# Kernel tuning notes

Measured on AMD Instinct MI355X. Metric: run time of the kernel, lower is better.

## Reference

```python
import jax, jax.numpy as jnp
import numpy as np

DIM = 192; HEADS = 6; WS = 8; SHIFT = 4; HID = int(DIM * 4.0)
CAB_SCALE = 0.01; COMPRESS = 3; SQUEEZE = 30
B = 8; H0 = 128; W0 = 128


def window_partition(x, ws):
    Bn, H, W, C = x.shape
    x = x.reshape(Bn, H // ws, ws, W // ws, ws, C).transpose(0, 1, 3, 2, 4, 5)
    return x.reshape(-1, ws, ws, C)


def window_reverse(w, ws, H, W):
    Bn = w.shape[0] // ((H // ws) * (W // ws))
    x = w.reshape(Bn, H // ws, W // ws, ws, ws, -1).transpose(0, 1, 3, 2, 4, 5)
    return x.reshape(Bn, H, W, -1)


def layernorm(x, w, b):
    mu = jnp.mean(x, -1, keepdims=True)
    var = jnp.var(x, -1, keepdims=True)
    return (x - mu) * jax.lax.rsqrt(var + 1e-5) * w + b


def conv3x3(x, w, b):
    y = jax.lax.conv_general_dilated(x, w, (1, 1), [(1, 1), (1, 1)],
                                     dimension_numbers=('NCHW', 'OIHW', 'NCHW'))
    return y + b[None, :, None, None]


def _coords_table(ws):
    # continuous relative coords table, log-spaced as in SwinV2
    r = np.arange(-(ws - 1), ws, dtype=np.float32)
    t = np.stack(np.meshgrid(r, r, indexing='ij'), -1) / (ws - 1) * 8.0
    t = np.sign(t) * np.log2(np.abs(t) + 1.0) / np.log2(8.0)
    return jnp.asarray(t.reshape(-1, 2))  # ((2ws-1)^2, 2)


def _rel_index(ws):
    c = np.stack(np.meshgrid(np.arange(ws), np.arange(ws), indexing='ij')).reshape(2, -1)
    r = (c[:, :, None] - c[:, None, :]).transpose(1, 2, 0)
    r[..., 0] += ws - 1; r[..., 1] += ws - 1; r[..., 0] *= 2 * ws - 1
    return jnp.asarray(r.sum(-1))  # (N, N) int


def _attn_mask(H, W, ws, shift):
    img = np.zeros((1, H, W, 1), np.float32); cnt = 0
    for hs in (slice(0, -ws), slice(-ws, -shift), slice(-shift, None)):
        for wsl in (slice(0, -ws), slice(-ws, -shift), slice(-shift, None)):
            img[:, hs, wsl, :] = cnt; cnt += 1
    win = img.reshape(1, H // ws, ws, W // ws, ws, 1).transpose(0, 1, 3, 2, 4, 5).reshape(-1, ws * ws)
    m = win[:, None, :] - win[:, :, None]
    return jnp.asarray(np.where(m != 0, -100.0, 0.0).astype(np.float32))  # (nW, N, N)


def _forward(x, norm1_w, norm1_b, qkv_w, q_bias, v_bias, logit_scale,
             cpb_w1, cpb_b1, cpb_w2, proj_w, proj_b,
             cab1_w, cab1_b, cab2_w, cab2_b, ca1_w, ca1_b, ca2_w, ca2_b,
             norm2_w, norm2_b, fc1_w, fc1_b, fc2_w, fc2_b, H, W):
    Bn, L, C = x.shape
    nh = HEADS; hd = C // nh; N = WS * WS
    shortcut = x
    xn = layernorm(x, norm1_w, norm1_b)
    xi = xn.reshape(Bn, H, W, C)

    # ---- CAB branch (Conv-GELU-Conv + channel attention) ----
    xc = xi.transpose(0, 3, 1, 2)                      # NCHW
    c = conv3x3(xc, cab1_w, cab1_b)
    c = jax.nn.gelu(c, approximate=False)
    c = conv3x3(c, cab2_w, cab2_b)
    s = c.mean((2, 3))                                 # (B, C) squeeze
    s = jax.nn.relu(s @ ca1_w.T + ca1_b)
    s = jax.nn.sigmoid(s @ ca2_w.T + ca2_b)
    conv_x = (c * s[:, :, None, None]).transpose(0, 2, 3, 1).reshape(Bn, L, C)

    # ---- shifted-window cosine attention ----
    xs = jnp.roll(xi, (-SHIFT, -SHIFT), axis=(1, 2)) if SHIFT > 0 else xi
    xw = window_partition(xs, WS).reshape(-1, N, C)    # (B*nW, N, C)
    qkv_bias = jnp.concatenate([q_bias, jnp.zeros_like(v_bias), v_bias])
    qkv = (xw @ qkv_w.T + qkv_bias).reshape(-1, N, 3, nh, hd).transpose(2, 0, 3, 1, 4)
    q, k, v = qkv[0], qkv[1], qkv[2]                   # (B_, nh, N, hd)
    qn = q / jnp.maximum(jnp.linalg.norm(q, axis=-1, keepdims=True), 1e-12)
    kn = k / jnp.maximum(jnp.linalg.norm(k, axis=-1, keepdims=True), 1e-12)
    attn = jnp.einsum('bhnd,bhmd->bhnm', qn, kn)
    scale = jnp.exp(jnp.minimum(logit_scale, jnp.log(100.0)))  # (nh,1,1)
    attn = attn * scale
    # CPB MLP relative position bias
    hbias = jax.nn.relu(_coords_table(WS) @ cpb_w1.T + cpb_b1) @ cpb_w2.T  # (T, nh)
    rpb = hbias[_rel_index(WS).reshape(-1)].reshape(N, N, nh).transpose(2, 0, 1)
    attn = attn + 16.0 * jax.nn.sigmoid(rpb)[None]
    if SHIFT > 0:
        mask = _attn_mask(H, W, WS, SHIFT)             # (nW, N, N)
        nW = mask.shape[0]
        attn = (attn.reshape(-1, nW, nh, N, N) + mask[None, :, None]).reshape(-1, nh, N, N)
    attn = jax.nn.softmax(attn, axis=-1)
    out = jnp.einsum('bhnm,bhmd->bhnd', attn, v).transpose(0, 2, 1, 3).reshape(-1, N, C)
    out = out @ proj_w.T + proj_b
    out = window_reverse(out.reshape(-1, WS, WS, C), WS, H, W)
    if SHIFT > 0:
        out = jnp.roll(out, (SHIFT, SHIFT), axis=(1, 2))
    attn_x = out.reshape(Bn, L, C)

    x = shortcut + attn_x + CAB_SCALE * conv_x
    h = layernorm(x, norm2_w, norm2_b)
    h = jax.nn.gelu(h @ fc1_w.T + fc1_b, approximate=False) @ fc2_w.T + fc2_b
    return x + h


def setup_inputs() -> dict:
    key = jax.random.key(0)
    ks = jax.random.split(key, 24)
    r = lambda k, shp, s=0.02: (jax.random.normal(k, shp, jnp.float32) * s)
    C = DIM; Cc = DIM // COMPRESS; Cs = DIM // SQUEEZE
    return {
        'x': jax.random.normal(ks[0], (B, H0 * W0, C), jnp.float32),
        'H': H0, 'W': W0,
        'norm1_w': jnp.ones((C,), jnp.float32), 'norm1_b': jnp.zeros((C,), jnp.float32),
        'qkv_w': r(ks[1], (3 * C, C)),
        'q_bias': jnp.zeros((C,), jnp.float32), 'v_bias': jnp.zeros((C,), jnp.float32),
        'logit_scale': jnp.full((HEADS, 1, 1), np.log(10.0), jnp.float32),
        'cpb_w1': r(ks[2], (512, 2), 0.1), 'cpb_b1': jnp.zeros((512,), jnp.float32),
        'cpb_w2': r(ks[3], (HEADS, 512), 0.1),
        'proj_w': r(ks[4], (C, C)), 'proj_b': jnp.zeros((C,), jnp.float32),
        'cab1_w': r(ks[5], (Cc, C, 3, 3)), 'cab1_b': jnp.zeros((Cc,), jnp.float32),
        'cab2_w': r(ks[6], (C, Cc, 3, 3)), 'cab2_b': jnp.zeros((C,), jnp.float32),
        'ca1_w': r(ks[7], (Cs, C)), 'ca1_b': jnp.zeros((Cs,), jnp.float32),
        'ca2_w': r(ks[8], (C, Cs)), 'ca2_b': jnp.zeros((C,), jnp.float32),
        'norm2_w': jnp.ones((C,), jnp.float32), 'norm2_b': jnp.zeros((C,), jnp.float32),
        'fc1_w': r(ks[9], (HID, C)), 'fc1_b': jnp.zeros((HID,), jnp.float32),
        'fc2_w': r(ks[10], (C, HID)), 'fc2_b': jnp.zeros((C,), jnp.float32),
    }


def reference(x, H, W, norm1_w, norm1_b, qkv_w, q_bias, v_bias, logit_scale,
              cpb_w1, cpb_b1, cpb_w2, proj_w, proj_b,
              cab1_w, cab1_b, cab2_w, cab2_b, ca1_w, ca1_b, ca2_w, ca2_b,
              norm2_w, norm2_b, fc1_w, fc1_b, fc2_w, fc2_b):
    return _forward(x, norm1_w, norm1_b, qkv_w, q_bias, v_bias, logit_scale,
                    cpb_w1, cpb_b1, cpb_w2, proj_w, proj_b,
                    cab1_w, cab1_b, cab2_w, cab2_b, ca1_w, ca1_b, ca2_w, ca2_b,
                    norm2_w, norm2_b, fc1_w, fc1_b, fc2_w, fc2_b, int(H), int(W))
```

## Files before the change

kernel.cpp:

```cpp
#include <hip/hip_runtime.h>
#include <math.h>


typedef unsigned short u16;
typedef __attribute__((ext_vector_type(8))) short short8;
typedef __attribute__((ext_vector_type(4))) float f32x4;

#define DI static __device__ __forceinline__

DI float b2f(u16 u){ union{unsigned u; float f;} v; v.u = ((unsigned)u)<<16; return v.f; }
DI u16 f2b(float f){ union{float f; unsigned u;} v; v.f = f; unsigned r = v.u + 0x7fffu + ((v.u>>16)&1u); return (u16)(r>>16); }
DI float gelu_f(float x){
  const float u = x*(0.7978845608f + 0.0356774081f*x*x);
  const float r = __builtin_amdgcn_rcpf(1.0f + __expf(2.0f*u));
  return x - x*r;
}

#define C2PLANE (12582912L)

__global__ __launch_bounds__(256) void ln_k(const float* __restrict__ in,
    const float* __restrict__ w, const float* __restrict__ b, u16* __restrict__ out)
{
  const int row  = blockIdx.x*4 + (threadIdx.x>>6);
  const int lane = threadIdx.x & 63;
  const float* r = in + (long)row*192;
  float v0 = r[lane], v1 = r[lane+64], v2 = r[lane+128];
  float s = v0+v1+v2;
  #pragma unroll
  for (int m=1;m<64;m<<=1) s += __shfl_xor(s, m);
  float mu = s*(1.0f/192.0f);
  float d0=v0-mu, d1=v1-mu, d2=v2-mu;
  float q = d0*d0+d1*d1+d2*d2;
  #pragma unroll
  for (int m=1;m<64;m<<=1) q += __shfl_xor(q, m);
  float rstd = rsqrtf(q*(1.0f/192.0f)+1e-5f);
  u16* o = out + (long)row*192;
  o[lane]     = f2b(d0*rstd*w[lane]    +b[lane]);
  o[lane+64]  = f2b(d1*rstd*w[lane+64] +b[lane+64]);
  o[lane+128] = f2b(d2*rstd*w[lane+128]+b[lane+128]);
}

__global__ __launch_bounds__(256) void prep_k(
    const float* __restrict__ qkv_w, const float* __restrict__ q_bias,
    const float* __restrict__ v_bias, const float* __restrict__ proj_w,
    const float* __restrict__ fc1_w, const float* __restrict__ fc2_w,
    const float* __restrict__ cab1_w, const float* __restrict__ cab2_w,
    const float* __restrict__ lgs,
    float* __restrict__ qkvbias, u16* __restrict__ wqkv, u16* __restrict__ wproj,
    u16* __restrict__ wfc1, u16* __restrict__ wfc2, u16* __restrict__ wt1,
    u16* __restrict__ wt2, float* __restrict__ scale6)
{
  int o = blockIdx.x*256 + threadIdx.x;
  if (o < 576){ qkvbias[o] = (o<192)? q_bias[o] : ((o<384)? 0.f : v_bias[o-384]); return; }
  o -= 576;
  if (o < 110592){ wqkv[o] = f2b(qkv_w[o]); return; } o -= 110592;
  if (o < 36864){
    const int e = o&7, lane = (o>>3)&63, ks = (o>>9)%6, nr = o/3072;
    const int row = nr*16 + (lane&15), col = ks*32 + (lane>>4)*8 + e;
    wproj[o] = f2b(proj_w[row*192 + col]); return; } o -= 36864;
  if (o < 147456){
    const int e = o&7, lane = (o>>3)&63, ks = (o>>9)%6, rest = o/3072;
    const int nr = rest&3, p = rest>>2;
    const int row = p*64 + nr*16 + (lane&15), col = ks*32 + (lane>>4)*8 + e;
    wfc1[o] = f2b(fc1_w[row*192 + col]); return; } o -= 147456;
  if (o < 147456){
    const int e = o&7, lane = (o>>3)&63, ks2 = (o>>9)&1, rest = o>>10;
    const int nr2 = rest%12, p = rest/12;
    const int row = nr2*16 + (lane&15);
    const int col = p*64 + ks2*32 + (lane>>4)*8 + e;
    wfc2[o] = f2b(fc2_w[row*768 + col]); return; } o -= 147456;
  if (o < 110592){
    int s = o/12288, r = o%12288, oc = r/192, ic = r%192, kh = s/3, kw = s%3;
    wt1[o] = f2b(cab1_w[((oc*192+ic)*3+kh)*3+kw]); return; } o -= 110592;
  if (o < 110592){
    int s = o/12288, r = o%12288, oc = r/64, ic = r%64, kh = s/3, kw = s%3;
    wt2[o] = f2b(cab2_w[((oc*64+ic)*3+kh)*3+kw]); return; } o -= 110592;
  if (o < 6){ scale6[o] = expf(fminf(lgs[o], logf(100.f))); }
}

__global__ __launch_bounds__(256) void rpb_k(const float* __restrict__ w1,
    const float* __restrict__ b1, const float* __restrict__ w2, float* __restrict__ rpbL)
{
  __shared__ float hb[225*6];
  const int tid = threadIdx.x;
  if (tid < 225){
    int di = tid/15, dj = tid%15;
    float vi = (di-7)*(8.0f/7.0f), vj = (dj-7)*(8.0f/7.0f);
    float t0 = (vi==0.f)?0.f:copysignf(log2f(fabsf(vi)+1.f)*(1.f/3.f), vi);
    float t1 = (vj==0.f)?0.f:copysignf(log2f(fabsf(vj)+1.f)*(1.f/3.f), vj);
    float acc[6] = {0,0,0,0,0,0};
    for (int hd=0; hd<512; ++hd){
      float a = fmaxf(t0*w1[hd*2] + t1*w1[hd*2+1] + b1[hd], 0.f);
      #pragma unroll
      for (int h=0;h<6;++h) acc[h] += a*w2[h*512+hd];
    }
    #pragma unroll
    for (int h=0;h<6;++h) hb[tid*6+h] = acc[h];
  }
  __syncthreads();
  for (int o = tid; o < 24576; o += 256){
    int i = o&3, lane = (o>>2)&63, mK = (o>>8)&3, nQ = (o>>10)&3, h = o>>12;
    int q = nQ*16 + (lane&15), k = mK*16 + (lane>>4)*4 + i;
    int idx = ((q>>3)-(k>>3)+7)*15 + ((q&7)-(k&7)+7);
    rpbL[o] = 16.0f/(1.0f+expf(-hb[idx*6+h]));
  }
}

template<int EPI, int KK, int NN>
__global__ __launch_bounds__(256) void gemm4_k(
    const u16* __restrict__ A, const u16* __restrict__ W,
    const float* __restrict__ bias, u16* __restrict__ outb)
{
  constexpr int NP = NN/64;
  __shared__ __align__(16) u16 As[128*200];
  __shared__ __align__(16) u16 Bs[64*200];
  const int tid = threadIdx.x, w = tid>>6, lane = tid&63;
  const int fr = lane&15, g = lane>>4;
  const int m0 = blockIdx.x*128;
  u16* obuf = Bs;

  #pragma unroll
  for (int i=0;i<12;++i){ const int id=tid+i*256, row=id/24, cc=id%24;
    *(short8*)&As[row*200+cc*8] =
      *(const short8*)(A + (long)(m0+row)*KK + cc*8); }

  short8 breg[6];
  #define LOADB(p) { \
    _Pragma("unroll") \
    for (int i=0;i<6;++i){ const int id=tid+i*256, br=id/24, cc=id%24; \
      breg[i] = *(const short8*)(W + (long)((p)*64+br)*KK + cc*8); } }
  #define STOREB() { \
    _Pragma("unroll") \
    for (int i=0;i<6;++i){ const int id=tid+i*256, br=id/24, cc=id%24; \
      *(short8*)&Bs[br*200+cc*8] = breg[i]; } }

  LOADB(0);
  for (int p=0; p<NP; ++p){
    __syncthreads();
    STOREB();
    __syncthreads();
    if (p+1 < NP) LOADB(p+1);
    f32x4 acc[2][4];
    #pragma unroll
    for (int a=0;a<2;++a)
      #pragma unroll
      for (int b=0;b<4;++b) acc[a][b] = (f32x4){0.f,0.f,0.f,0.f};
    #pragma unroll
    for (int ks=0; ks<6; ++ks){
      short8 af0 = *(const short8*)&As[(w*32+   fr)*200 + ks*32 + g*8];
      short8 af1 = *(const short8*)&As[(w*32+16+fr)*200 + ks*32 + g*8];
      #pragma unroll
      for (int nr=0;nr<4;++nr){
        short8 bf = *(const short8*)&Bs[(nr*16+fr)*200 + ks*32 + g*8];
        acc[0][nr] = __builtin_amdgcn_mfma_f32_16x16x32_bf16(af0, bf, acc[0][nr], 0,0,0);
        acc[1][nr] = __builtin_amdgcn_mfma_f32_16x16x32_bf16(af1, bf, acc[1][nr], 0,0,0);
      } }
    __syncthreads();
    #pragma unroll
    for (int mr=0;mr<2;++mr)
      #pragma unroll
      for (int nr=0;nr<4;++nr){
        const float bc = bias[p*64+nr*16+fr];
        #pragma unroll
        for (int i=0;i<4;++i){
          const int tok = w*32+mr*16+g*4+i;
          obuf[tok*72 + nr*16+fr] = f2b(acc[mr][nr][i] + bc); } }
    __syncthreads();
    #pragma unroll
    for (int j=0;j<4;++j){
      const int idx = tid + j*256, tok = idx>>3, cc = idx&7;
      *(short8*)(outb + (long)(m0+tok)*NN + p*64 + cc*8) =
          *(const short8*)&obuf[tok*72 + cc*8]; }
  }
  #undef LOADB
  #undef STOREB
}

__global__ __launch_bounds__(256) void proj_k(
    const u16* __restrict__ A, const u16* __restrict__ W,
    const float* __restrict__ bias, const float* __restrict__ resx,
    const u16* __restrict__ c2in, const float* __restrict__ sgate,
    float* __restrict__ outf)
{
  __shared__ __align__(16) u16 As[64*200];
  const int tid = threadIdx.x, w = tid>>6, lane = tid&63;
  const int fr = lane&15, g = lane>>4;
  const int m0 = blockIdx.x*64;

  #pragma unroll
  for (int i=0;i<6;++i){ const int id=tid+i*256, r=id/24, cc=id%24;
    *(short8*)&As[r*200+cc*8] = *(const short8*)(A + (long)(m0+r)*192 + cc*8); }
  __syncthreads();

  f32x4 acc[12];
  #pragma unroll
  for (int n=0;n<12;++n) acc[n] = (f32x4){0.f,0.f,0.f,0.f};
  #pragma unroll
  for (int ks=0;ks<6;++ks){
    const short8 af = *(const short8*)&As[(w*16+fr)*200 + ks*32 + g*8];
    #pragma unroll
    for (int nr=0;nr<12;++nr){
      const short8 bf = *(const short8*)(W + ((nr*6+ks)*64 + lane)*8);
      acc[nr] = __builtin_amdgcn_mfma_f32_16x16x32_bf16(af, bf, acc[nr], 0,0,0);
    }
  }

  float* fbuf = (float*)As;
  #pragma unroll
  for (int ch=0;ch<2;++ch){
    __syncthreads();
    #pragma unroll
    for (int nr=0;nr<6;++nr){
      const float bc = bias[ch*96 + nr*16 + fr];
      #pragma unroll
      for (int i=0;i<4;++i)
        fbuf[(w*16+g*4+i)*100 + nr*16+fr] = acc[ch*6+nr][i] + bc;
    }
    __syncthreads();
    #pragma unroll
    for (int j=0;j<6;++j){
      const int idx = tid + j*256, t = idx/24, cc = idx%24;
      const int tokg = m0 + t, gc0 = ch*96 + cc*4;
      const long o = (long)tokg*192 + gc0;
      f32x4 v = *(const f32x4*)&fbuf[t*100 + cc*4];
      const f32x4 r = *(const f32x4*)(resx + o);
      const u16* cp = c2in + (long)ch*C2PLANE + (long)tokg*96 + cc*4;
      const float* sg = sgate + (tokg>>14)*192 + gc0;
      #pragma unroll
      for (int e=0;e<4;++e) v[e] += r[e] + 0.01f*b2f(cp[e])*sg[e];
      *(f32x4*)(outf + o) = v;
    }
  }
}

__global__ __launch_bounds__(256, 2) void mlp_k(
    const float* __restrict__ xio,
    const float* __restrict__ lw, const float* __restrict__ lb,
    const u16* __restrict__ w1, const float* __restrict__ b1,
    const u16* __restrict__ w2, const float* __restrict__ b2,
    float* __restrict__ out)
{
  __shared__ __align__(16) char SB[25600];
  const int tid = threadIdx.x, w = tid>>6, lane = tid&63;
  const int fr = lane&15, g = lane>>4;
  const int m0 = blockIdx.x*128;
  u16* hs = ((u16*)SB) + w*(32*72);

  short8 af[2][6];
  #pragma unroll
  for (int mr=0; mr<2; ++mr){
    const long r = (long)(m0 + w*32 + mr*16 + fr)*192;
    f32x4 v[6][2];
    float s = 0.f;
    #pragma unroll
    for (int ks=0; ks<6; ++ks){
      v[ks][0] = *(const f32x4*)(xio + r + ks*32 + g*8);
      v[ks][1] = *(const f32x4*)(xio + r + ks*32 + g*8 + 4);
      #pragma unroll
      for (int e=0;e<4;++e) s += v[ks][0][e] + v[ks][1][e];
    }
    s += __shfl_xor(s,16); s += __shfl_xor(s,32);
    const float mu = s*(1.0f/192.0f);
    float q = 0.f;
    #pragma unroll
    for (int ks=0; ks<6; ++ks)
      #pragma unroll
      for (int h=0;h<2;++h)
        #pragma unroll
        for (int e=0;e<4;++e){ const float d = v[ks][h][e]-mu; q += d*d; }
    q += __shfl_xor(q,16); q += __shfl_xor(q,32);
    const float rstd = rsqrtf(q*(1.0f/192.0f)+1e-5f);
    #pragma unroll
    for (int ks=0; ks<6; ++ks){
      const int c0 = ks*32 + g*8;
      #pragma unroll
      for (int h=0;h<2;++h)
        #pragma unroll
        for (int e=0;e<4;++e)
          af[mr][ks][h*4+e] =
            (short)f2b((v[ks][h][e]-mu)*rstd*lw[c0+h*4+e] + lb[c0+h*4+e]);
    }
  }

  f32x4 acc2[2][12];
  #pragma unroll
  for (int a=0;a<2;++a)
    #pragma unroll
    for (int n=0;n<12;++n) acc2[a][n] = (f32x4){0.f,0.f,0.f,0.f};

  for (int p=0; p<12; ++p){
    f32x4 a1[2][4];
    #pragma unroll
    for (int a=0;a<2;++a)
      #pragma unroll
      for (int n=0;n<4;++n) a1[a][n] = (f32x4){0.f,0.f,0.f,0.f};
    #pragma unroll
    for (int ks=0;ks<6;++ks){
      #pragma unroll
      for (int nr=0;nr<4;++nr){
        const short8 bf = *(const short8*)(w1 + ((((p*4+nr)*6+ks)<<6) + lane)*8);
        a1[0][nr] = __builtin_amdgcn_mfma_f32_16x16x32_bf16(af[0][ks], bf, a1[0][nr], 0,0,0);
        a1[1][nr] = __builtin_amdgcn_mfma_f32_16x16x32_bf16(af[1][ks], bf, a1[1][nr], 0,0,0);
      }
    }
    #pragma unroll
    for (int mr=0;mr<2;++mr)
      #pragma unroll
      for (int nr=0;nr<4;++nr){
        const float bc = b1[p*64 + nr*16 + fr];
        #pragma unroll
        for (int i=0;i<4;++i)
          hs[(mr*16+g*4+i)*72 + nr*16+fr] = f2b(gelu_f(a1[mr][nr][i] + bc));
      }
    #pragma unroll
    for (int ks2=0;ks2<2;++ks2){
      const short8 ah0 = *(const short8*)&hs[(fr   )*72 + ks2*32 + g*8];
      const short8 ah1 = *(const short8*)&hs[(16+fr)*72 + ks2*32 + g*8];
      #pragma unroll
      for (int nr2=0;nr2<12;++nr2){
        const short8 bf = *(const short8*)(w2 + ((((p*12+nr2)*2+ks2)<<6) + lane)*8);
        acc2[0][nr2] = __builtin_amdgcn_mfma_f32_16x16x32_bf16(ah0, bf, acc2[0][nr2], 0,0,0);
        acc2[1][nr2] = __builtin_amdgcn_mfma_f32_16x16x32_bf16(ah1, bf, acc2[1][nr2], 0,0,0);
      }
    }
  }

  float* fbuf = (float*)SB;
  #pragma unroll
  for (int hp=0; hp<2; ++hp){
    #pragma unroll
    for (int ch=0;ch<2;++ch){
      __syncthreads();
      if ((w>>1) == hp){
        #pragma unroll
        for (int mr=0;mr<2;++mr)
          #pragma unroll
          for (int nr=0;nr<6;++nr){
            const float bc = b2[ch*96 + nr*16 + fr];
            #pragma unroll
            for (int i=0;i<4;++i)
              fbuf[((w&1)*32+mr*16+g*4+i)*100 + nr*16+fr] = acc2[mr][ch*6+nr][i] + bc;
          }
      }
      __syncthreads();
      #pragma unroll
      for (int j=0;j<6;++j){
        const int idx = tid + j*256, t = idx/24, cc = idx%24;
        const long o = (long)(m0 + hp*64 + t)*192 + ch*96 + cc*4;
        f32x4 v = *(const f32x4*)&fbuf[t*100 + cc*4];
        const f32x4 r = *(const f32x4*)(xio + o);
        #pragma unroll
        for (int e=0;e<4;++e) v[e] += r[e];
        *(f32x4*)(out + o) = v;
      }
    }
  }
}

template<int EPI, int CG, int IC, int OCT, int OCP, int NR, int TG>
__global__ __launch_bounds__(256, 2) void conv4_k(
    const u16* __restrict__ A, const u16* __restrict__ Wt,
    const float* __restrict__ bias, u16* __restrict__ outb,
    float* __restrict__ ssum)
{
  constexpr int NTG = 9/TG, S = CG*NTG;
  constexpr int WN = (TG*OCP*4 + 255)/256;
  __shared__ __align__(16) u16 Ah[4*130*36];
  __shared__ __align__(16) u16 Wl[TG*OCP*36];
  const int tid = threadIdx.x, w = tid>>6, lane = tid&63;
  const int fr = lane&15, g = lane>>4;
  const int b = blockIdx.x>>6, y0 = (blockIdx.x&63)*2;
  const int oc0 = blockIdx.y*OCP;
  const int wrow = w>>1, wcol = (w&1)*64;

  f32x4 acc[4][NR];
  #pragma unroll
  for (int a=0;a<4;++a)
    #pragma unroll
    for (int n=0;n<NR;++n) acc[a][n] = (f32x4){0.f,0.f,0.f,0.f};

  short8 hreg[8], wreg[WN];

  #define PRELOAD(s) { \
    const int cg_=(s)/NTG, tg_=(s)%NTG; \
    if (tg_==0){ \
      _Pragma("unroll") \
      for (int i=0;i<8;++i){ \
        const int id=tid+i*256, p=id>>9, x=(id>>2)&127, cc=id&3, y=y0+p-1; \
        short8 v={0,0,0,0,0,0,0,0}; \
        if ((unsigned)y<128u) \
          v = *(const short8*)(A + (long)((((b<<7)|y)<<7)|x)*IC + cg_*32 + cc*8); \
        hreg[i]=v; } } \
    _Pragma("unroll") \
    for (int i=0;i<WN;++i){ \
      const int id=tid+i*256; \
      if (id < TG*OCP*4){ \
        const int t=id/(OCP*4), r=id%(OCP*4), oc=r>>2, cc=r&3; \
        wreg[i] = *(const short8*)(Wt + \
            (long)((tg_*TG+t)*OCT + oc0 + oc)*IC + cg_*32 + cc*8); } } }

  #define STORE_STAGED(s) { \
    const int tg_=(s)%NTG; \
    if (tg_==0){ \
      _Pragma("unroll") \
      for (int i=0;i<8;++i){ \
        const int id=tid+i*256, p=id>>9, x=(id>>2)&127, cc=id&3; \
        *(short8*)&Ah[(p*130 + x + 1)*36 + cc*8] = hreg[i]; } \
      if (tid < 32){ \
        const int p=tid>>3, r=tid&7, col=(r>>2)?129:0, cc=r&3; \
        *(short8*)&Ah[(p*130 + col)*36 + cc*8] = (short8){0,0,0,0,0,0,0,0}; } } \
    _Pragma("unroll") \
    for (int i=0;i<WN;++i){ \
      const int id=tid+i*256; \
      if (id < TG*OCP*4){ \
        const int t=id/(OCP*4), r=id%(OCP*4), oc=r>>2, cc=r&3; \
        *(short8*)&Wl[(t*OCP+oc)*36 + cc*8] = wreg[i]; } } }

  #define COMPUTE(s) { \
    const int tg_=(s)%NTG; \
    _Pragma("unroll") \
    for (int t=0;t<TG;++t){ \
      const int tap=tg_*TG+t, dy=tap/3, dx=tap%3; \
      short8 bf[NR]; \
      _Pragma("unroll") \
      for (int nr=0;nr<NR;++nr) \
        bf[nr] = *(const short8*)&Wl[(t*OCP + nr*16 + fr)*36 + g*8]; \
      short8 af2[4]; \
      _Pragma("unroll") \
      for (int mr=0;mr<4;++mr) \
        af2[mr] = *(const short8*)&Ah[((wrow+dy)*130 + wcol + mr*16 + fr + dx)*36 + g*8]; \
      _Pragma("unroll") \
      for (int mr=0;mr<4;++mr) \
        _Pragma("unroll") \
        for (int nr=0;nr<NR;++nr) \
          acc[mr][nr] = __builtin_amdgcn_mfma_f32_16x16x32_bf16(af2[mr], bf[nr], acc[mr][nr], 0,0,0); } }

  PRELOAD(0);
  for (int s=0; s<S; ++s){
    __syncthreads();
    STORE_STAGED(s);
    __syncthreads();
    if (s+1 < S) PRELOAD(s+1);
    COMPUTE(s);
  }
  #undef PRELOAD
  #undef STORE_STAGED
  #undef COMPUTE

  if constexpr (EPI==2){
    #pragma unroll
    for (int nr=0;nr<NR;++nr){
      const float bc = bias[oc0 + nr*16 + fr];
      float s = 0.f;
      #pragma unroll
      for (int mr=0;mr<4;++mr)
        #pragma unroll
        for (int i=0;i<4;++i) s += acc[mr][nr][i] + bc;
      s += __shfl_xor(s,16); s += __shfl_xor(s,32);
      if (lane < 16) atomicAdd(&ssum[b*192 + oc0 + nr*16 + lane], s);
    }
  }

  u16* ob = Ah;
  const long tb = (long)(((b<<7)|y0)<<7);
  __syncthreads();
  if constexpr (EPI==1){
    #pragma unroll
    for (int mr=0;mr<4;++mr)
      #pragma unroll
      for (int nr=0;nr<NR;++nr){
        const float bc = bias[nr*16 + fr];
        #pragma unroll
        for (int i=0;i<4;++i){
          const int tok = wrow*128 + wcol + mr*16 + g*4 + i;
          ob[tok*72 + nr*16+fr] = f2b(gelu_f(acc[mr][nr][i] + bc));
        }
      }
    __syncthreads();
    #pragma unroll
    for (int j=0;j<8;++j){
      const int idx = tid + j*256, tok = idx>>3, cc = idx&7;
      *(short8*)(outb + (tb+tok)*OCP + cc*8) = *(const short8*)&ob[tok*72 + cc*8];
    }
  } else {
    const long pbase = (long)blockIdx.y*C2PLANE;
    #pragma unroll
    for (int h=0;h<2;++h){
      if (h) __syncthreads();
      if (wrow == h){
        #pragma unroll
        for (int mr=0;mr<4;++mr)
          #pragma unroll
          for (int nr=0;nr<NR;++nr){
            const float bc = bias[oc0 + nr*16 + fr];
            #pragma unroll
            for (int i=0;i<4;++i){
              const int tok = wcol + mr*16 + g*4 + i;
              ob[tok*104 + nr*16+fr] = f2b(acc[mr][nr][i] + bc);
            }
          }
      }
      __syncthreads();
      #pragma unroll
      for (int j=0;j<6;++j){
        const int idx = tid + j*256, t = idx/12, cc = idx%12;
        *(short8*)(outb + pbase + (tb + h*128 + t)*96 + cc*8) =
            *(const short8*)&ob[t*104 + cc*8];
      }
    }
  }
}

__global__ __launch_bounds__(256) void se_k(const float* __restrict__ ssum,
    const float* __restrict__ ca1w, const float* __restrict__ ca1b,
    const float* __restrict__ ca2w, const float* __restrict__ ca2b,
    float* __restrict__ sgate)
{
  __shared__ float hid[48];
  const int tid = threadIdx.x;
  if (tid < 48){
    int b = tid/6, cs = tid%6;
    float a = ca1b[cs];
    for (int c=0;c<192;++c) a += ssum[b*192+c]*(1.f/16384.f)*ca1w[cs*192+c];
    hid[tid] = fmaxf(a, 0.f);
  }
  __syncthreads();
  for (int o = tid; o < 1536; o += 256){
    int b = o/192, c = o%192;
    float a = ca2b[c];
    #pragma unroll
    for (int cs=0;cs<6;++cs) a += hid[b*6+cs]*ca2w[c*6+cs];
    sgate[o] = 1.f/(1.f+expf(-a));
  }
}

__global__ __launch_bounds__(256) void attn_k(const u16* __restrict__ qkv,
    const float* __restrict__ rpbL, const float* __restrict__ scale6,
    u16* __restrict__ aout)
{
  __shared__ int  lidx_s[4][64];
  __shared__ char region_s[4][64];
  __shared__ __align__(16) u16 p_s[4][64*72];
  const int tid = threadIdx.x, w = tid>>6, lane = tid&63;
  const int task = blockIdx.x*4 + w;
  const int win = task/6, h = task - win*6;
  const int b = win>>8, wn = win&255, wy = wn>>4, wx = wn&15;
  {
    int i = lane>>3, j = lane&7;
    int hs = wy*8+i, ws = wx*8+j;
    lidx_s[w][lane] = (b<<14) | (((hs+4)&127)<<7) | ((ws+4)&127);
    int hb = hs<120?0:(hs<124?1:2), wb = ws<120?0:(ws<124?1:2);
    region_s[w][lane] = (char)(hb*3+wb);
  }
  __syncthreads();
  const int g = lane>>4, l15 = lane&15;
  const bool edge = (wy==15) || (wx==15);
  const float scl = scale6[h];
  const f32x4 zf = {0.f,0.f,0.f,0.f};

  short8 kf[4];
  #pragma unroll
  for (int mt=0; mt<4; ++mt){
    const long base = (long)lidx_s[w][mt*16+l15]*576 + 192 + h*32 + g*8;
    short8 r = *(const short8*)(qkv + base);
    float f[8]; float ss = 0.f;
    #pragma unroll
    for (int e=0;e<8;++e){ f[e] = b2f((u16)r[e]); ss += f[e]*f[e]; }
    ss += __shfl_xor(ss,16); ss += __shfl_xor(ss,32);
    const float inv = 1.0f/fmaxf(sqrtf(ss), 1e-12f);
    #pragma unroll
    for (int e=0;e<8;++e) kf[mt][e] = (short)f2b(f[e]*inv);
  }

  #pragma unroll
  for (int nt=0; nt<4; ++nt){
    short8 qf;
    {
      const long base = (long)lidx_s[w][nt*16+l15]*576 + h*32 + g*8;
      short8 r = *(const short8*)(qkv + base);
      float f[8]; float ss = 0.f;
      #pragma unroll
      for (int e=0;e<8;++e){ f[e] = b2f((u16)r[e]); ss += f[e]*f[e]; }
      ss += __shfl_xor(ss,16); ss += __shfl_xor(ss,32);
      const float inv = 1.0f/fmaxf(sqrtf(ss), 1e-12f);
      #pragma unroll
      for (int e=0;e<8;++e) qf[e] = (short)f2b(f[e]*inv);
    }
    f32x4 st[4];
    #pragma unroll
    for (int mt=0; mt<4; ++mt)
      st[mt] = __builtin_amdgcn_mfma_f32_16x16x32_bf16(kf[mt], qf, zf, 0, 0, 0);
    float lv[16];
    const float* rp = rpbL + ((h*4+nt)*4)*256 + lane*4;
    const int rq = edge ? region_s[w][nt*16+l15] : 0;
    #pragma unroll
    for (int mt=0; mt<4; ++mt){
      const f32x4 rb = *(const f32x4*)(rp + mt*256);
      #pragma unroll
      for (int i=0;i<4;++i){
        float v = st[mt][i]*scl + rb[i];
        if (edge && region_s[w][mt*16+g*4+i] != rq) v -= 100.0f;
        lv[mt*4+i] = v;
      }
    }
    float mx = lv[0];
    #pragma unroll
    for (int t=1;t<16;++t) mx = fmaxf(mx, lv[t]);
    mx = fmaxf(mx, __shfl_xor(mx,16)); mx = fmaxf(mx, __shfl_xor(mx,32));
    float sum = 0.f;
    #pragma unroll
    for (int t=0;t<16;++t){ lv[t] = __expf(lv[t]-mx); sum += lv[t]; }
    sum += __shfl_xor(sum,16); sum += __shfl_xor(sum,32);
    const float isum = 1.0f/sum;
    u16* pr = p_s[w] + (nt*16+l15)*72;
    #pragma unroll
    for (int mt=0; mt<4; ++mt){
      #pragma unroll
      for (int j=0;j<2;++j){
        unsigned lo = f2b(lv[mt*4+2*j]  *isum);
        unsigned hi = f2b(lv[mt*4+2*j+1]*isum);
        *(unsigned*)(pr + mt*16 + g*4 + 2*j) = lo | (hi<<16);
      }
    }
  }

  short8 vf[2][2];
  #pragma unroll
  for (int nd=0; nd<2; ++nd)
    #pragma unroll
    for (int kc=0; kc<2; ++kc)
      #pragma unroll
      for (int e=0;e<8;++e){
        const int tok = kc*32 + g*8 + e;
        vf[nd][kc][e] = (short)qkv[(long)lidx_s[w][tok]*576 + 384 + h*32 + nd*16 + l15];
      }

  __syncthreads();

  #pragma unroll
  for (int mt=0; mt<4; ++mt){
    const short8 a0 = *(const short8*)(p_s[w] + (mt*16+l15)*72 +      g*8);
    const short8 a1 = *(const short8*)(p_s[w] + (mt*16+l15)*72 + 32 + g*8);
    #pragma unroll
    for (int nd=0; nd<2; ++nd){
      f32x4 o = __builtin_amdgcn_mfma_f32_16x16x32_bf16(a0, vf[nd][0], zf, 0, 0, 0);
      o = __builtin_amdgcn_mfma_f32_16x16x32_bf16(a1, vf[nd][1], o, 0, 0, 0);
      #pragma unroll
      for (int i=0;i<4;++i){
        const int q = mt*16 + g*4 + i;
        aout[(long)lidx_s[w][q]*192 + h*32 + nd*16 + l15] = f2b(o[i]);
      }
    }
  }
}

extern "C" void kernel_launch(void* const* d_in, const int* in_sizes, int n_in,
                              void* d_out, int out_size, void* d_ws, size_t ws_size,
                              hipStream_t stream)
{
  const float* x     = (const float*)d_in[0];
  const float* n1w   = (const float*)d_in[3];
  const float* n1b   = (const float*)d_in[4];
  const float* qkvw  = (const float*)d_in[5];
  const float* qb    = (const float*)d_in[6];
  const float* vb    = (const float*)d_in[7];
  const float* lgs   = (const float*)d_in[8];
  const float* cpb1w = (const float*)d_in[9];
  const float* cpb1b = (const float*)d_in[10];
  const float* cpb2w = (const float*)d_in[11];
  const float* projw = (const float*)d_in[12];
  const float* projb = (const float*)d_in[13];
  const float* cab1w = (const float*)d_in[14];
  const float* cab1b = (const float*)d_in[15];
  const float* cab2w = (const float*)d_in[16];
  const float* cab2b = (const float*)d_in[17];
  const float* ca1w  = (const float*)d_in[18];
  const float* ca1b  = (const float*)d_in[19];
  const float* ca2w  = (const float*)d_in[20];
  const float* ca2b  = (const float*)d_in[21];
  const float* n2w   = (const float*)d_in[22];
  const float* n2b   = (const float*)d_in[23];
  const float* fc1w  = (const float*)d_in[24];
  const float* fc1b  = (const float*)d_in[25];
  const float* fc2w  = (const float*)d_in[26];
  const float* fc2b  = (const float*)d_in[27];
  float* dout = (float*)d_out;
  char* ws = (char*)d_ws;

  constexpr size_t OFF_XN  = 0;
  constexpr size_t OFF_G1  = 50331648;
  constexpr size_t OFF_C2  = 67108864;
  constexpr size_t OFF_AO  = 167772160;
  constexpr size_t OFF_QKV = 218103808;
  constexpr size_t OFF_SM  = 369098752;

  u16*   xn      = (u16*)(ws + OFF_XN);
  u16*   g1      = (u16*)(ws + OFF_G1);
  u16*   c2      = (u16*)(ws + OFF_C2);
  u16*   ao      = (u16*)(ws + OFF_AO);
  u16*   qkvb    = (u16*)(ws + OFF_QKV);
  float* qkvbias = (float*)(ws + OFF_SM);
  float* scale6  = (float*)(ws + OFF_SM + 4096);
  float* ssum    = (float*)(ws + OFF_SM + 8192);
  float* sgate   = (float*)(ws + OFF_SM + 16384);
  float* rpbL    = (float*)(ws + OFF_SM + 24576);
  u16*   wqkv    = (u16*)(ws + OFF_SM + 131072);
  u16*   wproj   = (u16*)(ws + OFF_SM + 360448);
  u16*   wfc1    = (u16*)(ws + OFF_SM + 434176);
  u16*   wfc2    = (u16*)(ws + OFF_SM + 729088);
  u16*   wt1     = (u16*)(ws + OFF_SM + 1024000);
  u16*   wt2     = (u16*)(ws + OFF_SM + 1245184);

  prep_k<<<2595, 256, 0, stream>>>(qkvw, qb, vb, projw, fc1w, fc2w, cab1w, cab2w,
                                   lgs, qkvbias, wqkv, wproj, wfc1, wfc2, wt1, wt2, scale6);
  rpb_k<<<1, 256, 0, stream>>>(cpb1w, cpb1b, cpb2w, rpbL);
  ln_k<<<32768, 256, 0, stream>>>(x, n1w, n1b, xn);
  hipMemsetAsync(ssum, 0, 1536*4, stream);
  conv4_k<1,6,192,64,64,4,9><<<dim3(512,1), 256, 0, stream>>>(xn, wt1, cab1b, g1, nullptr);
  conv4_k<2,2,64,192,96,6,3><<<dim3(512,2), 256, 0, stream>>>(g1, wt2, cab2b, c2, ssum);
  se_k<<<1, 256, 0, stream>>>(ssum, ca1w, ca1b, ca2w, ca2b, sgate);
  gemm4_k<0,192,576><<<1024, 256, 0, stream>>>(xn, wqkv, qkvbias, qkvb);
  attn_k<<<3072, 256, 0, stream>>>(qkvb, rpbL, scale6, ao);
  proj_k<<<2048, 256, 0, stream>>>(ao, wproj, projb, x, c2, sgate, dout);
  mlp_k<<<1024, 256, 0, stream>>>(dout, n2w, n2b, wfc1, fc1b, wfc2, fc2b, dout);
}
```

Before: 636.3 us.

## Merge independent kernels into horizontally fused launches by block-index dispatch

Combines the layernorm, weight prep and relative-position-bias kernels into one launch, and folds the ssum memset into it. The first conv and the QKV GEMM now share one launch, as do attention and the second conv, with each block choosing its work from its block index. This removes launch gaps and lets independent branches overlap on the GPU. In exchange, the fused kernels take the largest shared-memory footprint and register budget of their members, which can lower occupancy for the lighter parts such as attention. Correctness still relies on the rpb block zeroing ssum before stage3's conv atomics, which the launch order provides.

```diff
diff --git a/kernel.cpp b/kernel.cpp
--- a/kernel.cpp
+++ b/kernel.cpp
@@ -18,11 +18,13 @@
 
 #define C2PLANE (12582912L)
 
-__global__ __launch_bounds__(256) void ln_k(const float* __restrict__ in,
-    const float* __restrict__ w, const float* __restrict__ b, u16* __restrict__ out)
-{
-  const int row  = blockIdx.x*4 + (threadIdx.x>>6);
-  const int lane = threadIdx.x & 63;
+
+DI void ln_body(int bid, int tid, const float* __restrict__ in,
+                const float* __restrict__ w, const float* __restrict__ b,
+                u16* __restrict__ out)
+{
+  const int row  = bid*4 + (tid>>6);
+  const int lane = tid & 63;
   const float* r = in + (long)row*192;
   float v0 = r[lane], v1 = r[lane+64], v2 = r[lane+128];
   float s = v0+v1+v2;
@@ -40,7 +42,7 @@
   o[lane+128] = f2b(d2*rstd*w[lane+128]+b[lane+128]);
 }
 
-__global__ __launch_bounds__(256) void prep_k(
+DI void prep_body(int bid, int tid,
     const float* __restrict__ qkv_w, const float* __restrict__ q_bias,
     const float* __restrict__ v_bias, const float* __restrict__ proj_w,
     const float* __restrict__ fc1_w, const float* __restrict__ fc2_w,
@@ -50,7 +52,7 @@
     u16* __restrict__ wfc1, u16* __restrict__ wfc2, u16* __restrict__ wt1,
     u16* __restrict__ wt2, float* __restrict__ scale6)
 {
-  int o = blockIdx.x*256 + threadIdx.x;
+  int o = bid*256 + tid;
   if (o < 576){ qkvbias[o] = (o<192)? q_bias[o] : ((o<384)? 0.f : v_bias[o-384]); return; }
   o -= 576;
   if (o < 110592){ wqkv[o] = f2b(qkv_w[o]); return; } o -= 110592;
@@ -78,11 +80,12 @@
   if (o < 6){ scale6[o] = expf(fminf(lgs[o], logf(100.f))); }
 }
 
-__global__ __launch_bounds__(256) void rpb_k(const float* __restrict__ w1,
-    const float* __restrict__ b1, const float* __restrict__ w2, float* __restrict__ rpbL)
-{
-  __shared__ float hb[225*6];
-  const int tid = threadIdx.x;
+DI void rpb_body(int tid, float* hb,
+    const float* __restrict__ w1, const float* __restrict__ b1,
+    const float* __restrict__ w2, float* __restrict__ rpbL,
+    float* __restrict__ ssum)
+{
+  for (int i=tid; i<1536; i+=256) ssum[i] = 0.f;
   if (tid < 225){
     int di = tid/15, dj = tid%15;
     float vi = (di-7)*(8.0f/7.0f), vj = (dj-7)*(8.0f/7.0f);
@@ -106,17 +109,17 @@
   }
 }
 
-template<int EPI, int KK, int NN>
-__global__ __launch_bounds__(256) void gemm4_k(
+template<int KK, int NN>
+DI void gemm4_body(char* LDSU, int bid, int tid,
     const u16* __restrict__ A, const u16* __restrict__ W,
     const float* __restrict__ bias, u16* __restrict__ outb)
 {
   constexpr int NP = NN/64;
-  __shared__ __align__(16) u16 As[128*200];
-  __shared__ __align__(16) u16 Bs[64*200];
-  const int tid = threadIdx.x, w = tid>>6, lane = tid&63;
+  u16* As = (u16*)LDSU;
+  u16* Bs = (u16*)(LDSU + 102400);
+  const int w = tid>>6, lane = tid&63;
   const int fr = lane&15, g = lane>>4;
-  const int m0 = blockIdx.x*128;
+  const int m0 = bid*128;
   u16* obuf = Bs;
 
   #pragma unroll
@@ -176,201 +179,20 @@
   #undef STOREB
 }
 
-__global__ __launch_bounds__(256) void proj_k(
-    const u16* __restrict__ A, const u16* __restrict__ W,
-    const float* __restrict__ bias, const float* __restrict__ resx,
-    const u16* __restrict__ c2in, const float* __restrict__ sgate,
-    float* __restrict__ outf)
-{
-  __shared__ __align__(16) u16 As[64*200];
-  const int tid = threadIdx.x, w = tid>>6, lane = tid&63;
-  const int fr = lane&15, g = lane>>4;
-  const int m0 = blockIdx.x*64;
-
-  #pragma unroll
-  for (int i=0;i<6;++i){ const int id=tid+i*256, r=id/24, cc=id%24;
-    *(short8*)&As[r*200+cc*8] = *(const short8*)(A + (long)(m0+r)*192 + cc*8); }
-  __syncthreads();
-
-  f32x4 acc[12];
-  #pragma unroll
-  for (int n=0;n<12;++n) acc[n] = (f32x4){0.f,0.f,0.f,0.f};
-  #pragma unroll
-  for (int ks=0;ks<6;++ks){
-    const short8 af = *(const short8*)&As[(w*16+fr)*200 + ks*32 + g*8];
-    #pragma unroll
-    for (int nr=0;nr<12;++nr){
-      const short8 bf = *(const short8*)(W + ((nr*6+ks)*64 + lane)*8);
-      acc[nr] = __builtin_amdgcn_mfma_f32_16x16x32_bf16(af, bf, acc[nr], 0,0,0);
-    }
-  }
-
-  float* fbuf = (float*)As;
-  #pragma unroll
-  for (int ch=0;ch<2;++ch){
-    __syncthreads();
-    #pragma unroll
-    for (int nr=0;nr<6;++nr){
-      const float bc = bias[ch*96 + nr*16 + fr];
-      #pragma unroll
-      for (int i=0;i<4;++i)
-        fbuf[(w*16+g*4+i)*100 + nr*16+fr] = acc[ch*6+nr][i] + bc;
-    }
-    __syncthreads();
-    #pragma unroll
-    for (int j=0;j<6;++j){
-      const int idx = tid + j*256, t = idx/24, cc = idx%24;
-      const int tokg = m0 + t, gc0 = ch*96 + cc*4;
-      const long o = (long)tokg*192 + gc0;
-      f32x4 v = *(const f32x4*)&fbuf[t*100 + cc*4];
-      const f32x4 r = *(const f32x4*)(resx + o);
-      const u16* cp = c2in + (long)ch*C2PLANE + (long)tokg*96 + cc*4;
-      const float* sg = sgate + (tokg>>14)*192 + gc0;
-      #pragma unroll
-      for (int e=0;e<4;++e) v[e] += r[e] + 0.01f*b2f(cp[e])*sg[e];
-      *(f32x4*)(outf + o) = v;
-    }
-  }
-}
-
-__global__ __launch_bounds__(256, 2) void mlp_k(
-    const float* __restrict__ xio,
-    const float* __restrict__ lw, const float* __restrict__ lb,
-    const u16* __restrict__ w1, const float* __restrict__ b1,
-    const u16* __restrict__ w2, const float* __restrict__ b2,
-    float* __restrict__ out)
-{
-  __shared__ __align__(16) char SB[25600];
-  const int tid = threadIdx.x, w = tid>>6, lane = tid&63;
-  const int fr = lane&15, g = lane>>4;
-  const int m0 = blockIdx.x*128;
-  u16* hs = ((u16*)SB) + w*(32*72);
-
-  short8 af[2][6];
-  #pragma unroll
-  for (int mr=0; mr<2; ++mr){
-    const long r = (long)(m0 + w*32 + mr*16 + fr)*192;
-    f32x4 v[6][2];
-    float s = 0.f;
-    #pragma unroll
-    for (int ks=0; ks<6; ++ks){
-      v[ks][0] = *(const f32x4*)(xio + r + ks*32 + g*8);
-      v[ks][1] = *(const f32x4*)(xio + r + ks*32 + g*8 + 4);
-      #pragma unroll
-      for (int e=0;e<4;++e) s += v[ks][0][e] + v[ks][1][e];
-    }
-    s += __shfl_xor(s,16); s += __shfl_xor(s,32);
-    const float mu = s*(1.0f/192.0f);
-    float q = 0.f;
-    #pragma unroll
-    for (int ks=0; ks<6; ++ks)
-      #pragma unroll
-      for (int h=0;h<2;++h)
-        #pragma unroll
-        for (int e=0;e<4;++e){ const float d = v[ks][h][e]-mu; q += d*d; }
-    q += __shfl_xor(q,16); q += __shfl_xor(q,32);
-    const float rstd = rsqrtf(q*(1.0f/192.0f)+1e-5f);
-    #pragma unroll
-    for (int ks=0; ks<6; ++ks){
-      const int c0 = ks*32 + g*8;
-      #pragma unroll
-      for (int h=0;h<2;++h)
-        #pragma unroll
-        for (int e=0;e<4;++e)
-          af[mr][ks][h*4+e] =
-            (short)f2b((v[ks][h][e]-mu)*rstd*lw[c0+h*4+e] + lb[c0+h*4+e]);
-    }
-  }
-
-  f32x4 acc2[2][12];
-  #pragma unroll
-  for (int a=0;a<2;++a)
-    #pragma unroll
-    for (int n=0;n<12;++n) acc2[a][n] = (f32x4){0.f,0.f,0.f,0.f};
-
-  for (int p=0; p<12; ++p){
-    f32x4 a1[2][4];
-    #pragma unroll
-    for (int a=0;a<2;++a)
-      #pragma unroll
-      for (int n=0;n<4;++n) a1[a][n] = (f32x4){0.f,0.f,0.f,0.f};
-    #pragma unroll
-    for (int ks=0;ks<6;++ks){
-      #pragma unroll
-      for (int nr=0;nr<4;++nr){
-        const short8 bf = *(const short8*)(w1 + ((((p*4+nr)*6+ks)<<6) + lane)*8);
-        a1[0][nr] = __builtin_amdgcn_mfma_f32_16x16x32_bf16(af[0][ks], bf, a1[0][nr], 0,0,0);
-        a1[1][nr] = __builtin_amdgcn_mfma_f32_16x16x32_bf16(af[1][ks], bf, a1[1][nr], 0,0,0);
-      }
-    }
-    #pragma unroll
-    for (int mr=0;mr<2;++mr)
-      #pragma unroll
-      for (int nr=0;nr<4;++nr){
-        const float bc = b1[p*64 + nr*16 + fr];
-        #pragma unroll
-        for (int i=0;i<4;++i)
-          hs[(mr*16+g*4+i)*72 + nr*16+fr] = f2b(gelu_f(a1[mr][nr][i] + bc));
-      }
-    #pragma unroll
-    for (int ks2=0;ks2<2;++ks2){
-      const short8 ah0 = *(const short8*)&hs[(fr   )*72 + ks2*32 + g*8];
-      const short8 ah1 = *(const short8*)&hs[(16+fr)*72 + ks2*32 + g*8];
-      #pragma unroll
-      for (int nr2=0;nr2<12;++nr2){
-        const short8 bf = *(const short8*)(w2 + ((((p*12+nr2)*2+ks2)<<6) + lane)*8);
-        acc2[0][nr2] = __builtin_amdgcn_mfma_f32_16x16x32_bf16(ah0, bf, acc2[0][nr2], 0,0,0);
-        acc2[1][nr2] = __builtin_amdgcn_mfma_f32_16x16x32_bf16(ah1, bf, acc2[1][nr2], 0,0,0);
-      }
-    }
-  }
-
-  float* fbuf = (float*)SB;
-  #pragma unroll
-  for (int hp=0; hp<2; ++hp){
-    #pragma unroll
-    for (int ch=0;ch<2;++ch){
-      __syncthreads();
-      if ((w>>1) == hp){
-        #pragma unroll
-        for (int mr=0;mr<2;++mr)
-          #pragma unroll
-          for (int nr=0;nr<6;++nr){
-            const float bc = b2[ch*96 + nr*16 + fr];
-            #pragma unroll
-            for (int i=0;i<4;++i)
-              fbuf[((w&1)*32+mr*16+g*4+i)*100 + nr*16+fr] = acc2[mr][ch*6+nr][i] + bc;
-          }
-      }
-      __syncthreads();
-      #pragma unroll
-      for (int j=0;j<6;++j){
-        const int idx = tid + j*256, t = idx/24, cc = idx%24;
-        const long o = (long)(m0 + hp*64 + t)*192 + ch*96 + cc*4;
-        f32x4 v = *(const f32x4*)&fbuf[t*100 + cc*4];
-        const f32x4 r = *(const f32x4*)(xio + o);
-        #pragma unroll
-        for (int e=0;e<4;++e) v[e] += r[e];
-        *(f32x4*)(out + o) = v;
-      }
-    }
-  }
-}
-
 template<int EPI, int CG, int IC, int OCT, int OCP, int NR, int TG>
-__global__ __launch_bounds__(256, 2) void conv4_k(
+DI void conv4_body(char* LDSU, int bx, int by, int tid,
     const u16* __restrict__ A, const u16* __restrict__ Wt,
     const float* __restrict__ bias, u16* __restrict__ outb,
     float* __restrict__ ssum)
 {
   constexpr int NTG = 9/TG, S = CG*NTG;
   constexpr int WN = (TG*OCP*4 + 255)/256;
-  __shared__ __align__(16) u16 Ah[4*130*36];
-  __shared__ __align__(16) u16 Wl[TG*OCP*36];
-  const int tid = threadIdx.x, w = tid>>6, lane = tid&63;
+  u16* Ah = (u16*)LDSU;
+  u16* Wl = (u16*)(LDSU + 37440);
+  const int w = tid>>6, lane = tid&63;
   const int fr = lane&15, g = lane>>4;
-  const int b = blockIdx.x>>6, y0 = (blockIdx.x&63)*2;
-  const int oc0 = blockIdx.y*OCP;
+  const int b = bx>>6, y0 = (bx&63)*2;
+  const int oc0 = by*OCP;
   const int wrow = w>>1, wcol = (w&1)*64;
 
   f32x4 acc[4][NR];
@@ -483,7 +305,7 @@
       *(short8*)(outb + (tb+tok)*OCP + cc*8) = *(const short8*)&ob[tok*72 + cc*8];
     }
   } else {
-    const long pbase = (long)blockIdx.y*C2PLANE;
+    const long pbase = (long)by*C2PLANE;
     #pragma unroll
     for (int h=0;h<2;++h){
       if (h) __syncthreads();
@@ -511,6 +333,187 @@
   }
 }
 
+DI void attn_body(char* LDSU, int bid, int tid,
+    const u16* __restrict__ qkv, const float* __restrict__ rpbL,
+    const float* __restrict__ scale6, u16* __restrict__ aout)
+{
+  int*  lidx_s   = (int*)LDSU;
+  char* region_s = LDSU + 1024;
+  u16*  p_sb     = (u16*)(LDSU + 1280);
+  const int w = tid>>6, lane = tid&63;
+  const int task = bid*4 + w;
+  const int win = task/6, h = task - win*6;
+  const int b = win>>8, wn = win&255, wy = wn>>4, wx = wn&15;
+  {
+    int i = lane>>3, j = lane&7;
+    int hs = wy*8+i, ws = wx*8+j;
+    lidx_s[w*64+lane] = (b<<14) | (((hs+4)&127)<<7) | ((ws+4)&127);
+    int hb = hs<120?0:(hs<124?1:2), wb = ws<120?0:(ws<124?1:2);
+    region_s[w*64+lane] = (char)(hb*3+wb);
+  }
+  __syncthreads();
+  const int g = lane>>4, l15 = lane&15;
+  const int* lidx = lidx_s + w*64;
+  const char* region = region_s + w*64;
+  u16* p_s = p_sb + w*4608;
+  const bool edge = (wy==15) || (wx==15);
+  const float scl = scale6[h];
+  const f32x4 zf = {0.f,0.f,0.f,0.f};
+
+  short8 kf[4];
+  #pragma unroll
+  for (int mt=0; mt<4; ++mt){
+    const long base = (long)lidx[mt*16+l15]*576 + 192 + h*32 + g*8;
+    short8 r = *(const short8*)(qkv + base);
+    float f[8]; float ss = 0.f;
+    #pragma unroll
+    for (int e=0;e<8;++e){ f[e] = b2f((u16)r[e]); ss += f[e]*f[e]; }
+    ss += __shfl_xor(ss,16); ss += __shfl_xor(ss,32);
+    const float inv = 1.0f/fmaxf(sqrtf(ss), 1e-12f);
+    #pragma unroll
+    for (int e=0;e<8;++e) kf[mt][e] = (short)f2b(f[e]*inv);
+  }
+
+  #pragma unroll
+  for (int nt=0; nt<4; ++nt){
+    short8 qf;
+    {
+      const long base = (long)lidx[nt*16+l15]*576 + h*32 + g*8;
+      short8 r = *(const short8*)(qkv + base);
+      float f[8]; float ss = 0.f;
+      #pragma unroll
+      for (int e=0;e<8;++e){ f[e] = b2f((u16)r[e]); ss += f[e]*f[e]; }
+      ss += __shfl_xor(ss,16); ss += __shfl_xor(ss,32);
+      const float inv = 1.0f/fmaxf(sqrtf(ss), 1e-12f);
+      #pragma unroll
+      for (int e=0;e<8;++e) qf[e] = (short)f2b(f[e]*inv);
+    }
+    f32x4 st[4];
+    #pragma unroll
+    for (int mt=0; mt<4; ++mt)
+      st[mt] = __builtin_amdgcn_mfma_f32_16x16x32_bf16(kf[mt], qf, zf, 0, 0, 0);
+    float lv[16];
+    const float* rp = rpbL + ((h*4+nt)*4)*256 + lane*4;
+    const int rq = edge ? region[nt*16+l15] : 0;
+    #pragma unroll
+    for (int mt=0; mt<4; ++mt){
+      const f32x4 rb = *(const f32x4*)(rp + mt*256);
+      #pragma unroll
+      for (int i=0;i<4;++i){
+        float v = st[mt][i]*scl + rb[i];
+        if (edge && region[mt*16+g*4+i] != rq) v -= 100.0f;
+        lv[mt*4+i] = v;
+      }
+    }
+    float mx = lv[0];
+    #pragma unroll
+    for (int t=1;t<16;++t) mx = fmaxf(mx, lv[t]);
+    mx = fmaxf(mx, __shfl_xor(mx,16)); mx = fmaxf(mx, __shfl_xor(mx,32));
+    float sum = 0.f;
+    #pragma unroll
+    for (int t=0;t<16;++t){ lv[t] = __expf(lv[t]-mx); sum += lv[t]; }
+    sum += __shfl_xor(sum,16); sum += __shfl_xor(sum,32);
+    const float isum = 1.0f/sum;
+    u16* pr = p_s + (nt*16+l15)*72;
+    #pragma unroll
+    for (int mt=0; mt<4; ++mt){
+      #pragma unroll
+      for (int j=0;j<2;++j){
+        unsigned lo = f2b(lv[mt*4+2*j]  *isum);
+        unsigned hi = f2b(lv[mt*4+2*j+1]*isum);
+        *(unsigned*)(pr + mt*16 + g*4 + 2*j) = lo | (hi<<16);
+      }
+    }
+  }
+
+  short8 vf[2][2];
+  #pragma unroll
+  for (int nd=0; nd<2; ++nd)
+    #pragma unroll
+    for (int kc=0; kc<2; ++kc)
+      #pragma unroll
+      for (int e=0;e<8;++e){
+        const int tok = kc*32 + g*8 + e;
+        vf[nd][kc][e] = (short)qkv[(long)lidx[tok]*576 + 384 + h*32 + nd*16 + l15];
+      }
+
+  __syncthreads();
+
+  #pragma unroll
+  for (int mt=0; mt<4; ++mt){
+    const short8 a0 = *(const short8*)(p_s + (mt*16+l15)*72 +      g*8);
+    const short8 a1 = *(const short8*)(p_s + (mt*16+l15)*72 + 32 + g*8);
+    #pragma unroll
+    for (int nd=0; nd<2; ++nd){
+      f32x4 o = __builtin_amdgcn_mfma_f32_16x16x32_bf16(a0, vf[nd][0], zf, 0, 0, 0);
+      o = __builtin_amdgcn_mfma_f32_16x16x32_bf16(a1, vf[nd][1], o, 0, 0, 0);
+      #pragma unroll
+      for (int i=0;i<4;++i){
+        const int q = mt*16 + g*4 + i;
+        aout[(long)lidx[q]*192 + h*32 + nd*16 + l15] = f2b(o[i]);
+      }
+    }
+  }
+}
+
+
+__global__ __launch_bounds__(256) void setup_k(
+    const float* __restrict__ x, const float* __restrict__ n1w,
+    const float* __restrict__ n1b, u16* __restrict__ xn,
+    const float* __restrict__ qkvw, const float* __restrict__ qb,
+    const float* __restrict__ vb, const float* __restrict__ projw,
+    const float* __restrict__ fc1w, const float* __restrict__ fc2w,
+    const float* __restrict__ cab1w, const float* __restrict__ cab2w,
+    const float* __restrict__ lgs,
+    float* __restrict__ qkvbias, u16* __restrict__ wqkv, u16* __restrict__ wproj,
+    u16* __restrict__ wfc1, u16* __restrict__ wfc2, u16* __restrict__ wt1,
+    u16* __restrict__ wt2, float* __restrict__ scale6,
+    const float* __restrict__ cpb1w, const float* __restrict__ cpb1b,
+    const float* __restrict__ cpb2w, float* __restrict__ rpbL,
+    float* __restrict__ ssum)
+{
+  __shared__ float hb[1350];
+  const int bid = blockIdx.x, tid = threadIdx.x;
+  if (bid < 32768){ ln_body(bid, tid, x, n1w, n1b, xn); return; }
+  if (bid < 35363){
+    prep_body(bid-32768, tid, qkvw, qb, vb, projw, fc1w, fc2w, cab1w, cab2w,
+              lgs, qkvbias, wqkv, wproj, wfc1, wfc2, wt1, wt2, scale6);
+    return;
+  }
+  rpb_body(tid, hb, cpb1w, cpb1b, cpb2w, rpbL, ssum);
+}
+
+__global__ __launch_bounds__(256, 2) void stage2_k(
+    const u16* __restrict__ xn, const u16* __restrict__ wt1,
+    const float* __restrict__ cab1b, u16* __restrict__ g1,
+    const u16* __restrict__ wqkv, const float* __restrict__ qkvbias,
+    u16* __restrict__ qkvb)
+{
+  __shared__ __align__(16) char LDSU[128000];
+  const int bid = blockIdx.x, tid = threadIdx.x;
+  if (bid < 512)
+    conv4_body<1,6,192,64,64,4,9>(LDSU, bid, 0, tid, xn, wt1, cab1b, g1, nullptr);
+  else
+    gemm4_body<192,576>(LDSU, bid-512, tid, xn, wqkv, qkvbias, qkvb);
+}
+
+__global__ __launch_bounds__(256, 2) void stage3_k(
+    const u16* __restrict__ qkvb, const float* __restrict__ rpbL,
+    const float* __restrict__ scale6, u16* __restrict__ ao,
+    const u16* __restrict__ g1, const u16* __restrict__ wt2,
+    const float* __restrict__ cab2b, u16* __restrict__ c2,
+    float* __restrict__ ssum)
+{
+  __shared__ __align__(16) char LDSU[58176];
+  const int bid = blockIdx.x, tid = threadIdx.x;
+  if (bid < 3072)
+    attn_body(LDSU, bid, tid, qkvb, rpbL, scale6, ao);
+  else {
+    const int b2 = bid - 3072;
+    conv4_body<2,2,64,192,96,6,3>(LDSU, b2 & 511, b2 >> 9, tid, g1, wt2, cab2b, c2, ssum);
+  }
+}
+
 __global__ __launch_bounds__(256) void se_k(const float* __restrict__ ssum,
     const float* __restrict__ ca1w, const float* __restrict__ ca1b,
     const float* __restrict__ ca2w, const float* __restrict__ ca2b,
@@ -534,121 +537,182 @@
   }
 }
 
-__global__ __launch_bounds__(256) void attn_k(const u16* __restrict__ qkv,
-    const float* __restrict__ rpbL, const float* __restrict__ scale6,
-    u16* __restrict__ aout)
-{
-  __shared__ int  lidx_s[4][64];
-  __shared__ char region_s[4][64];
-  __shared__ __align__(16) u16 p_s[4][64*72];
+__global__ __launch_bounds__(256) void proj_k(
+    const u16* __restrict__ A, const u16* __restrict__ W,
+    const float* __restrict__ bias, const float* __restrict__ resx,
+    const u16* __restrict__ c2in, const float* __restrict__ sgate,
+    float* __restrict__ outf)
+{
+  __shared__ __align__(16) u16 As[64*200];
   const int tid = threadIdx.x, w = tid>>6, lane = tid&63;
-  const int task = blockIdx.x*4 + w;
-  const int win = task/6, h = task - win*6;
-  const int b = win>>8, wn = win&255, wy = wn>>4, wx = wn&15;
-  {
-    int i = lane>>3, j = lane&7;
-    int hs = wy*8+i, ws = wx*8+j;
-    lidx_s[w][lane] = (b<<14) | (((hs+4)&127)<<7) | ((ws+4)&127);
-    int hb = hs<120?0:(hs<124?1:2), wb = ws<120?0:(ws<124?1:2);
-    region_s[w][lane] = (char)(hb*3+wb);
-  }
+  const int fr = lane&15, g = lane>>4;
+  const int m0 = blockIdx.x*64;
+
+  #pragma unroll
+  for (int i=0;i<6;++i){ const int id=tid+i*256, r=id/24, cc=id%24;
+    *(short8*)&As[r*200+cc*8] = *(const short8*)(A + (long)(m0+r)*192 + cc*8); }
   __syncthreads();
-  const int g = lane>>4, l15 = lane&15;
-  const bool edge = (wy==15) || (wx==15);
-  const float scl = scale6[h];
-  const f32x4 zf = {0.f,0.f,0.f,0.f};
-
-  short8 kf[4];
-  #pragma unroll
-  for (int mt=0; mt<4; ++mt){
-    const long base = (long)lidx_s[w][mt*16+l15]*576 + 192 + h*32 + g*8;
-    short8 r = *(const short8*)(qkv + base);
-    float f[8]; float ss = 0.f;
-    #pragma unroll
-    for (int e=0;e<8;++e){ f[e] = b2f((u16)r[e]); ss += f[e]*f[e]; }
-    ss += __shfl_xor(ss,16); ss += __shfl_xor(ss,32);
-    const float inv = 1.0f/fmaxf(sqrtf(ss), 1e-12f);
-    #pragma unroll
-    for (int e=0;e<8;++e) kf[mt][e] = (short)f2b(f[e]*inv);
-  }
-
-  #pragma unroll
-  for (int nt=0; nt<4; ++nt){
-    short8 qf;
-    {
-      const long base = (long)lidx_s[w][nt*16+l15]*576 + h*32 + g*8;
-      short8 r = *(const short8*)(qkv + base);
-      float f[8]; float ss = 0.f;
-      #pragma unroll
-      for (int e=0;e<8;++e){ f[e] = b2f((u16)r[e]); ss += f[e]*f[e]; }
-      ss += __shfl_xor(ss,16); ss += __shfl_xor(ss,32);
-      const float inv = 1.0f/fmaxf(sqrtf(ss), 1e-12f);
-      #pragma unroll
-      for (int e=0;e<8;++e) qf[e] = (short)f2b(f[e]*inv);
-    }
-    f32x4 st[4];
-    #pragma unroll
-    for (int mt=0; mt<4; ++mt)
-      st[mt] = __builtin_amdgcn_mfma_f32_16x16x32_bf16(kf[mt], qf, zf, 0, 0, 0);
-    float lv[16];
-    const float* rp = rpbL + ((h*4+nt)*4)*256 + lane*4;
-    const int rq = edge ? region_s[w][nt*16+l15] : 0;
-    #pragma unroll
-    for (int mt=0; mt<4; ++mt){
-      const f32x4 rb = *(const f32x4*)(rp + mt*256);
-      #pragma unroll
-      for (int i=0;i<4;++i){
-        float v = st[mt][i]*scl + rb[i];
-        if (edge && region_s[w][mt*16+g*4+i] != rq) v -= 100.0f;
-        lv[mt*4+i] = v;
-      }
-    }
-    float mx = lv[0];
-    #pragma unroll
-    for (int t=1;t<16;++t) mx = fmaxf(mx, lv[t]);
-    mx = fmaxf(mx, __shfl_xor(mx,16)); mx = fmaxf(mx, __shfl_xor(mx,32));
-    float sum = 0.f;
-    #pragma unroll
-    for (int t=0;t<16;++t){ lv[t] = __expf(lv[t]-mx); sum += lv[t]; }
-    sum += __shfl_xor(sum,16); sum += __shfl_xor(sum,32);
-    const float isum = 1.0f/sum;
-    u16* pr = p_s[w] + (nt*16+l15)*72;
-    #pragma unroll
-    for (int mt=0; mt<4; ++mt){
-      #pragma unroll
-      for (int j=0;j<2;++j){
-        unsigned lo = f2b(lv[mt*4+2*j]  *isum);
-        unsigned hi = f2b(lv[mt*4+2*j+1]*isum);
-        *(unsigned*)(pr + mt*16 + g*4 + 2*j) = lo | (hi<<16);
-      }
-    }
-  }
-
-  short8 vf[2][2];
-  #pragma unroll
-  for (int nd=0; nd<2; ++nd)
-    #pragma unroll
-    for (int kc=0; kc<2; ++kc)
-      #pragma unroll
-      for (int e=0;e<8;++e){
-        const int tok = kc*32 + g*8 + e;
-        vf[nd][kc][e] = (short)qkv[(long)lidx_s[w][tok]*576 + 384 + h*32 + nd*16 + l15];
-      }
-
-  __syncthreads();
-
-  #pragma unroll
-  for (int mt=0; mt<4; ++mt){
-    const short8 a0 = *(const short8*)(p_s[w] + (mt*16+l15)*72 +      g*8);
-    const short8 a1 = *(const short8*)(p_s[w] + (mt*16+l15)*72 + 32 + g*8);
-    #pragma unroll
-    for (int nd=0; nd<2; ++nd){
-      f32x4 o = __builtin_amdgcn_mfma_f32_16x16x32_bf16(a0, vf[nd][0], zf, 0, 0, 0);
-      o = __builtin_amdgcn_mfma_f32_16x16x32_bf16(a1, vf[nd][1], o, 0, 0, 0);
-      #pragma unroll
-      for (int i=0;i<4;++i){
-        const int q = mt*16 + g*4 + i;
-        aout[(long)lidx_s[w][q]*192 + h*32 + nd*16 + l15] = f2b(o[i]);
+
+  f32x4 acc[12];
+  #pragma unroll
+  for (int n=0;n<12;++n) acc[n] = (f32x4){0.f,0.f,0.f,0.f};
+  #pragma unroll
+  for (int ks=0;ks<6;++ks){
+    const short8 af = *(const short8*)&As[(w*16+fr)*200 + ks*32 + g*8];
+    #pragma unroll
+    for (int nr=0;nr<12;++nr){
+      const short8 bf = *(const short8*)(W + ((nr*6+ks)*64 + lane)*8);
+      acc[nr] = __builtin_amdgcn_mfma_f32_16x16x32_bf16(af, bf, acc[nr], 0,0,0);
+    }
+  }
+
+  float* fbuf = (float*)As;
+  #pragma unroll
+  for (int ch=0;ch<2;++ch){
+    __syncthreads();
+    #pragma unroll
+    for (int nr=0;nr<6;++nr){
+      const float bc = bias[ch*96 + nr*16 + fr];
+      #pragma unroll
+      for (int i=0;i<4;++i)
+        fbuf[(w*16+g*4+i)*100 + nr*16+fr] = acc[ch*6+nr][i] + bc;
+    }
+    __syncthreads();
+    #pragma unroll
+    for (int j=0;j<6;++j){
+      const int idx = tid + j*256, t = idx/24, cc = idx%24;
+      const int tokg = m0 + t, gc0 = ch*96 + cc*4;
+      const long o = (long)tokg*192 + gc0;
+      f32x4 v = *(const f32x4*)&fbuf[t*100 + cc*4];
+      const f32x4 r = *(const f32x4*)(resx + o);
+      const u16* cp = c2in + (long)ch*C2PLANE + (long)tokg*96 + cc*4;
+      const float* sg = sgate + (tokg>>14)*192 + gc0;
+      #pragma unroll
+      for (int e=0;e<4;++e) v[e] += r[e] + 0.01f*b2f(cp[e])*sg[e];
+      *(f32x4*)(outf + o) = v;
+    }
+  }
+}
+
+__global__ __launch_bounds__(256, 2) void mlp_k(
+    const float* __restrict__ xio,
+    const float* __restrict__ lw, const float* __restrict__ lb,
+    const u16* __restrict__ w1, const float* __restrict__ b1,
+    const u16* __restrict__ w2, const float* __restrict__ b2,
+    float* __restrict__ out)
+{
+  __shared__ __align__(16) char SB[25600];
+  const int tid = threadIdx.x, w = tid>>6, lane = tid&63;
+  const int fr = lane&15, g = lane>>4;
+  const int m0 = blockIdx.x*128;
+  u16* hs = ((u16*)SB) + w*(32*72);
+
+  short8 af[2][6];
+  #pragma unroll
+  for (int mr=0; mr<2; ++mr){
+    const long r = (long)(m0 + w*32 + mr*16 + fr)*192;
+    f32x4 v[6][2];
+    float s = 0.f;
+    #pragma unroll
+    for (int ks=0; ks<6; ++ks){
+      v[ks][0] = *(const f32x4*)(xio + r + ks*32 + g*8);
+      v[ks][1] = *(const f32x4*)(xio + r + ks*32 + g*8 + 4);
+      #pragma unroll
+      for (int e=0;e<4;++e) s += v[ks][0][e] + v[ks][1][e];
+    }
+    s += __shfl_xor(s,16); s += __shfl_xor(s,32);
+    const float mu = s*(1.0f/192.0f);
+    float q = 0.f;
+    #pragma unroll
+    for (int ks=0; ks<6; ++ks)
+      #pragma unroll
+      for (int h=0;h<2;++h)
+        #pragma unroll
+        for (int e=0;e<4;++e){ const float d = v[ks][h][e]-mu; q += d*d; }
+    q += __shfl_xor(q,16); q += __shfl_xor(q,32);
+    const float rstd = rsqrtf(q*(1.0f/192.0f)+1e-5f);
+    #pragma unroll
+    for (int ks=0; ks<6; ++ks){
+      const int c0 = ks*32 + g*8;
+      #pragma unroll
+      for (int h=0;h<2;++h)
+        #pragma unroll
+        for (int e=0;e<4;++e)
+          af[mr][ks][h*4+e] =
+            (short)f2b((v[ks][h][e]-mu)*rstd*lw[c0+h*4+e] + lb[c0+h*4+e]);
+    }
+  }
+
+  f32x4 acc2[2][12];
+  #pragma unroll
+  for (int a=0;a<2;++a)
+    #pragma unroll
+    for (int n=0;n<12;++n) acc2[a][n] = (f32x4){0.f,0.f,0.f,0.f};
+
+  for (int p=0; p<12; ++p){
+    f32x4 a1[2][4];
+    #pragma unroll
+    for (int a=0;a<2;++a)
+      #pragma unroll
+      for (int n=0;n<4;++n) a1[a][n] = (f32x4){0.f,0.f,0.f,0.f};
+    #pragma unroll
+    for (int ks=0;ks<6;++ks){
+      #pragma unroll
+      for (int nr=0;nr<4;++nr){
+        const short8 bf = *(const short8*)(w1 + ((((p*4+nr)*6+ks)<<6) + lane)*8);
+        a1[0][nr] = __builtin_amdgcn_mfma_f32_16x16x32_bf16(af[0][ks], bf, a1[0][nr], 0,0,0);
+        a1[1][nr] = __builtin_amdgcn_mfma_f32_16x16x32_bf16(af[1][ks], bf, a1[1][nr], 0,0,0);
+      }
+    }
+    #pragma unroll
+    for (int mr=0;mr<2;++mr)
+      #pragma unroll
+      for (int nr=0;nr<4;++nr){
+        const float bc = b1[p*64 + nr*16 + fr];
+        #pragma unroll
+        for (int i=0;i<4;++i)
+          hs[(mr*16+g*4+i)*72 + nr*16+fr] = f2b(gelu_f(a1[mr][nr][i] + bc));
+      }
+    #pragma unroll
+    for (int ks2=0;ks2<2;++ks2){
+      const short8 ah0 = *(const short8*)&hs[(fr   )*72 + ks2*32 + g*8];
+      const short8 ah1 = *(const short8*)&hs[(16+fr)*72 + ks2*32 + g*8];
+      #pragma unroll
+      for (int nr2=0;nr2<12;++nr2){
+        const short8 bf = *(const short8*)(w2 + ((((p*12+nr2)*2+ks2)<<6) + lane)*8);
+        acc2[0][nr2] = __builtin_amdgcn_mfma_f32_16x16x32_bf16(ah0, bf, acc2[0][nr2], 0,0,0);
+        acc2[1][nr2] = __builtin_amdgcn_mfma_f32_16x16x32_bf16(ah1, bf, acc2[1][nr2], 0,0,0);
+      }
+    }
+  }
+
+  float* fbuf = (float*)SB;
+  #pragma unroll
+  for (int hp=0; hp<2; ++hp){
+    #pragma unroll
+    for (int ch=0;ch<2;++ch){
+      __syncthreads();
+      if ((w>>1) == hp){
+        #pragma unroll
+        for (int mr=0;mr<2;++mr)
+          #pragma unroll
+          for (int nr=0;nr<6;++nr){
+            const float bc = b2[ch*96 + nr*16 + fr];
+            #pragma unroll
+            for (int i=0;i<4;++i)
+              fbuf[((w&1)*32+mr*16+g*4+i)*100 + nr*16+fr] = acc2[mr][ch*6+nr][i] + bc;
+          }
+      }
+      __syncthreads();
+      #pragma unroll
+      for (int j=0;j<6;++j){
+        const int idx = tid + j*256, t = idx/24, cc = idx%24;
+        const long o = (long)(m0 + hp*64 + t)*192 + ch*96 + cc*4;
+        f32x4 v = *(const f32x4*)&fbuf[t*100 + cc*4];
+        const f32x4 r = *(const f32x4*)(xio + o);
+        #pragma unroll
+        for (int e=0;e<4;++e) v[e] += r[e];
+        *(f32x4*)(out + o) = v;
       }
     }
   }
@@ -711,16 +775,13 @@
   u16*   wt1     = (u16*)(ws + OFF_SM + 1024000);
   u16*   wt2     = (u16*)(ws + OFF_SM + 1245184);
 
-  prep_k<<<2595, 256, 0, stream>>>(qkvw, qb, vb, projw, fc1w, fc2w, cab1w, cab2w,
-                                   lgs, qkvbias, wqkv, wproj, wfc1, wfc2, wt1, wt2, scale6);
-  rpb_k<<<1, 256, 0, stream>>>(cpb1w, cpb1b, cpb2w, rpbL);
-  ln_k<<<32768, 256, 0, stream>>>(x, n1w, n1b, xn);
-  hipMemsetAsync(ssum, 0, 1536*4, stream);
-  conv4_k<1,6,192,64,64,4,9><<<dim3(512,1), 256, 0, stream>>>(xn, wt1, cab1b, g1, nullptr);
-  conv4_k<2,2,64,192,96,6,3><<<dim3(512,2), 256, 0, stream>>>(g1, wt2, cab2b, c2, ssum);
+  setup_k<<<35364, 256, 0, stream>>>(x, n1w, n1b, xn,
+      qkvw, qb, vb, projw, fc1w, fc2w, cab1w, cab2w, lgs,
+      qkvbias, wqkv, wproj, wfc1, wfc2, wt1, wt2, scale6,
+      cpb1w, cpb1b, cpb2w, rpbL, ssum);
+  stage2_k<<<1536, 256, 0, stream>>>(xn, wt1, cab1b, g1, wqkv, qkvbias, qkvb);
+  stage3_k<<<4096, 256, 0, stream>>>(qkvb, rpbL, scale6, ao, g1, wt2, cab2b, c2, ssum);
   se_k<<<1, 256, 0, stream>>>(ssum, ca1w, ca1b, ca2w, ca2b, sgate);
-  gemm4_k<0,192,576><<<1024, 256, 0, stream>>>(xn, wqkv, qkvbias, qkvb);
-  attn_k<<<3072, 256, 0, stream>>>(qkvb, rpbL, scale6, ao);
   proj_k<<<2048, 256, 0, stream>>>(ao, wproj, projb, x, c2, sgate, dout);
   mlp_k<<<1024, 256, 0, stream>>>(dout, n2w, n2b, wfc1, fc1b, wfc2, fc2b, dout);
 }
```

Result: slower. 832.6 us (+30.9%).
